# Performance work log

Measured on AMD Instinct MI355X. Metric: run time of the kernel, lower is better.

Reference implementation:

```python
import jax, jax.numpy as jnp
import numpy as np
import math

D = 384        # d_model
DC = 1024      # d_cut3r
NH = 8         # n_heads
NP = 4         # n_points
B, H, W = 8, 64, 64
EPS = 1e-5


def _offset_bias():
    thetas = np.arange(NH) * (2.0 * math.pi / NH)
    g = np.stack([np.cos(thetas), np.sin(thetas)], -1)
    g = g / np.abs(g).max(-1, keepdims=True)
    g = np.tile(g[:, None, :], (1, NP, 1)) * ((np.arange(NP) + 1.0) / NP)[None, :, None]
    return jnp.asarray(g.reshape(-1), jnp.float32)


def _ln(x, g, b):
    m = x.mean(-1, keepdims=True)
    v = ((x - m) ** 2).mean(-1, keepdims=True)
    return (x - m) * jax.lax.rsqrt(v + EPS) * g + b


def _grid_sample(img, grid):
    # img: [N, C, Hk, Wk]; grid: [N, Q, P, 2] with (x, y) in [-1, 1]
    # torch F.grid_sample semantics: bilinear, padding_mode='zeros', align_corners=False
    N, C, Hk, Wk = img.shape
    ix = ((grid[..., 0] + 1.0) * Wk - 1.0) * 0.5   # [N,Q,P] pixel coords
    iy = ((grid[..., 1] + 1.0) * Hk - 1.0) * 0.5
    x0 = jnp.floor(ix); y0 = jnp.floor(iy)
    wx1 = ix - x0; wx0 = 1.0 - wx1
    wy1 = iy - y0; wy0 = 1.0 - wy1
    flat = img.reshape(N, C, Hk * Wk)

    def corner(xf, yf, wgt):
        valid = (xf >= 0) & (xf < Wk) & (yf >= 0) & (yf < Hk)
        xi = jnp.clip(xf, 0, Wk - 1).astype(jnp.int32)
        yi = jnp.clip(yf, 0, Hk - 1).astype(jnp.int32)
        idx = (yi * Wk + xi).reshape(N, 1, -1)  # [N,1,Q*P]
        v = jnp.take_along_axis(flat, jnp.broadcast_to(idx, (N, C, idx.shape[-1])), axis=2)
        v = v.reshape(N, C, xf.shape[1], xf.shape[2])               # [N,C,Q,P]
        w = (wgt * valid.astype(img.dtype))[:, None]                # [N,1,Q,P]
        return v * w

    return (corner(x0, y0, wx0 * wy0) + corner(x0 + 1.0, y0, wx1 * wy0)
            + corner(x0, y0 + 1.0, wx0 * wy1) + corner(x0 + 1.0, y0 + 1.0, wx1 * wy1))


def setup_inputs() -> dict:
    key = jax.random.key(0)
    ks = jax.random.split(key, 16)
    rn = lambda k, shape: jax.random.normal(k, shape, jnp.float32) * 0.02
    return {
        'visual_feat': jax.random.normal(ks[0], (B, D, H, W), jnp.float32),
        'cut3r_features': jax.random.normal(ks[1], (B, 730, DC), jnp.float32),
        'ln_v_g': jnp.ones((D,), jnp.float32), 'ln_v_b': jnp.zeros((D,), jnp.float32),
        'ln_c_g': jnp.ones((DC,), jnp.float32), 'ln_c_b': jnp.zeros((DC,), jnp.float32),
        'W_c1': rn(ks[2], (DC, 2 * D)), 'b_c1': jnp.zeros((2 * D,), jnp.float32),
        'W_c2': rn(ks[3], (2 * D, D)), 'b_c2': jnp.zeros((D,), jnp.float32),
        'W_off': rn(ks[4], (D, NH * NP * 2)), 'b_off': _offset_bias(),
        'W_attn': rn(ks[5], (D, NH * NP)), 'b_attn': jnp.zeros((NH * NP,), jnp.float32),
        'W_out': rn(ks[6], (D, D)), 'b_out': jnp.zeros((D,), jnp.float32),
        'W_f1': rn(ks[7], (D, 4 * D)), 'b_f1': jnp.zeros((4 * D,), jnp.float32),
        'W_f2': rn(ks[8], (4 * D, D)), 'b_f2': jnp.zeros((D,), jnp.float32),
        'W_g1': rn(ks[9], (D, D // 4)), 'b_g1': jnp.zeros((D // 4,), jnp.float32),
        'W_g2': rn(ks[10], (D // 4, 1)), 'b_g2': jnp.full((1,), -5.0, jnp.float32),
        'ln_o_g': jnp.ones((D,), jnp.float32), 'ln_o_b': jnp.zeros((D,), jnp.float32),
    }


def reference(visual_feat, cut3r_features, ln_v_g, ln_v_b, ln_c_g, ln_c_b,
              W_c1, b_c1, W_c2, b_c2, W_off, b_off, W_attn, b_attn,
              W_out, b_out, W_f1, b_f1, W_f2, b_f2, W_g1, b_g1, W_g2, b_g2,
              ln_o_g, ln_o_b):
    Bb, C, Hh, Ww = visual_feat.shape
    Nq = Hh * Ww
    dh = C // NH
    vflat = visual_feat.reshape(Bb, C, Nq).transpose(0, 2, 1)            # [B,Nq,C]
    vn = _ln(vflat, ln_v_g, ln_v_b)
    cn = _ln(cut3r_features, ln_c_g, ln_c_b)
    cp = jax.nn.gelu(cn @ W_c1 + b_c1, approximate=False) @ W_c2 + b_c2  # [B,730,C]
    grid = cp[:, 1:, :].reshape(Bb, 27, 27, C).transpose(0, 3, 1, 2)     # [B,C,27,27]
    off = (vn @ W_off + b_off).reshape(Bb, Nq, NH, NP, 2)
    aw = jax.nn.softmax((vn @ W_attn + b_attn).reshape(Bb, Nq, NH, NP), axis=-1)
    loc = 2.0 * jax.nn.sigmoid(off) - 1.0                                # [-1,1]
    loc = loc.transpose(0, 2, 1, 3, 4).reshape(Bb * NH, Nq, NP, 2)
    value = grid.reshape(Bb * NH, dh, 27, 27)
    samp = _grid_sample(value, loc).reshape(Bb, NH, dh, Nq, NP)
    out = (samp * aw.transpose(0, 2, 1, 3)[:, :, None]).sum(-1)          # [B,NH,dh,Nq]
    out = out.transpose(0, 3, 1, 2).reshape(Bb, Nq, C)
    attn_out = out @ W_out + b_out
    ffn = jax.nn.gelu(attn_out @ W_f1 + b_f1, approximate=False) @ W_f2 + b_f2
    gate = jax.nn.sigmoid(jax.nn.relu(vflat @ W_g1 + b_g1) @ W_g2 + b_g2)  # [B,Nq,1]
    fused = _ln(vflat + gate * ffn, ln_o_g, ln_o_b)
    fused = fused.transpose(0, 2, 1).reshape(Bb, C, Hh, Ww)
    return fused, gate
```

## Files before the change

kernel.cpp:

```cpp
#include <hip/hip_runtime.h>
#include <hip/hip_bf16.h>
#include <math.h>

#define B_   8
#define D_   384
#define DC_  1024
#define NH_  8
#define NP_  4
#define DH_  48
#define NQ_  4096
#define NT_  730
#define NG_  729
#define GW_  27

typedef unsigned short u16;
typedef __attribute__((ext_vector_type(8))) short s8bf;
typedef __attribute__((ext_vector_type(4))) float f32x4;

__device__ __forceinline__ float bf2f(u16 u) { return __uint_as_float(((unsigned)u) << 16); }
__device__ __forceinline__ u16 f2bf(float f) {
    __hip_bfloat16 h = __float2bfloat16(f);
    return *reinterpret_cast<u16*>(&h);
}
__device__ __forceinline__ float rd(const float* p) { return *p; }
__device__ __forceinline__ float rd(const u16* p)   { return bf2f(*p); }
__device__ __forceinline__ void  wr(float* p, float v) { *p = v; }
__device__ __forceinline__ void  wr(u16* p, float v)   { *p = f2bf(v); }
__device__ __forceinline__ void fmacc4(float4& o, const float4 v, float w) {
    o.x = fmaf(v.x, w, o.x); o.y = fmaf(v.y, w, o.y);
    o.z = fmaf(v.z, w, o.z); o.w = fmaf(v.w, w, o.w);
}
__device__ __forceinline__ int imin(int a, int b) { return a < b ? a : b; }
__device__ __forceinline__ float fast_gelu(float x) {
    float z = 1.5957691216057308f * fmaf(0.044715f * x, x * x, x);
    return x / (1.f + __expf(-z));
}
__device__ __forceinline__ float fast_sigmoid(float x) {
    return 1.f / (1.f + __expf(-x));
}

#define GLOAD16(gp, lp) \
    __builtin_amdgcn_global_load_lds( \
        (const __attribute__((address_space(1))) void*)(gp), \
        (__attribute__((address_space(3))) void*)(lp), 16, 0, 0)

__global__ __launch_bounds__(256) void tr_ln_kernel(
    const float* __restrict__ visual,
    const float* __restrict__ g, const float* __restrict__ be,
    u16* __restrict__ vflat, u16* __restrict__ vn)
{
    __shared__ float lds[D_][33];
    __shared__ float sM[32], sR[32];
    const int blk = blockIdx.x;
    const int b = blk >> 7, q0 = (blk & 127) << 5;
    const int t = threadIdx.x;
    const int tx = t & 31, ty = t >> 5;
    const float* vb = visual + (size_t)b * D_ * NQ_ + q0;
#pragma unroll
    for (int ct = 0; ct < 12; ++ct)
#pragma unroll
        for (int i = 0; i < 32; i += 8) {
            const int c = ct * 32 + ty + i;
            lds[c][tx] = vb[(size_t)c * NQ_ + tx];
        }
    __syncthreads();
    const int wv = t >> 6, lane = t & 63;
    for (int k = 0; k < 8; ++k) {
        const int q = wv * 8 + k;
        float s = 0.f, ss = 0.f;
#pragma unroll
        for (int e = 0; e < 6; ++e) {
            float v = lds[lane * 6 + e][q];
            s += v; ss += v * v;
        }
#pragma unroll
        for (int o = 32; o > 0; o >>= 1) { s += __shfl_down(s, o); ss += __shfl_down(ss, o); }
        if (lane == 0) {
            float m = s / (float)D_;
            sM[q] = m; sR[q] = rsqrtf(ss / (float)D_ - m * m + 1e-5f);
        }
    }
    __syncthreads();
    for (int idx = t; idx < 32 * D_; idx += 256) {
        const int q = idx / D_, c = idx % D_;
        const float raw = lds[c][q];
        const size_t row = (size_t)b * NQ_ + q0 + q;
        vflat[row * D_ + c] = f2bf(raw);
        vn[row * D_ + c]    = f2bf((raw - sM[q]) * sR[q] * g[c] + be[c]);
    }
}

__global__ __launch_bounds__(256) void fused_ln_tr_kernel(
    const u16* __restrict__ vflat, const float* __restrict__ gate,
    const u16* __restrict__ ffn,
    const float* __restrict__ g, const float* __restrict__ be,
    float* __restrict__ outT)
{
    __shared__ float buf[D_][33];
    __shared__ float sM[32], sR[32], sG[32];
    const int blk = blockIdx.x;
    const int b = blk >> 7, q0 = (blk & 127) << 5;
    const int t = threadIdx.x;
    const int tx = t & 31, ty = t >> 5;
    if (t < 32) sG[t] = gate[(size_t)b * NQ_ + q0 + t];
    __syncthreads();
    for (int idx = t; idx < 32 * D_; idx += 256) {
        const int q = idx / D_, c = idx % D_;
        const size_t row = (size_t)b * NQ_ + q0 + q;
        buf[c][q] = bf2f(vflat[row * D_ + c]) + sG[q] * bf2f(ffn[row * D_ + c]);
    }
    __syncthreads();
    const int wv = t >> 6, lane = t & 63;
    for (int k = 0; k < 8; ++k) {
        const int q = wv * 8 + k;
        float s = 0.f, ss = 0.f;
#pragma unroll
        for (int e = 0; e < 6; ++e) {
            float v = buf[lane * 6 + e][q];
            s += v; ss += v * v;
        }
#pragma unroll
        for (int o = 32; o > 0; o >>= 1) { s += __shfl_down(s, o); ss += __shfl_down(ss, o); }
        if (lane == 0) {
            float m = s / (float)D_;
            sM[q] = m; sR[q] = rsqrtf(ss / (float)D_ - m * m + 1e-5f);
        }
    }
    __syncthreads();
    float* ob = outT + (size_t)b * D_ * NQ_ + q0;
#pragma unroll
    for (int ct = 0; ct < 12; ++ct)
#pragma unroll
        for (int i = 0; i < 32; i += 8) {
            const int c = ct * 32 + ty + i;
            ob[(size_t)c * NQ_ + tx] = (buf[c][tx] - sM[tx]) * sR[tx] * g[c] + be[c];
        }
}

struct WtD { const float* src; u16* dst; int R; int C; int start; };
struct WtArgs { WtD d[8]; };

__global__ __launch_bounds__(256) void wt_convert_kernel(WtArgs a)
{
    __shared__ float tile[32][33];
    const int bt = blockIdx.x;
    int wi = 0;
#pragma unroll
    for (int k = 1; k < 8; ++k) if (bt >= a.d[k].start) wi = k;
    const float* src = a.d[wi].src;
    u16*         dst = a.d[wi].dst;
    const int R = a.d[wi].R, C = a.d[wi].C;
    const int local = bt - a.d[wi].start;
    const int tilesX = C >> 5;
    const int c0 = (local % tilesX) << 5;
    const int r0 = (local / tilesX) << 5;
    const int tx = threadIdx.x & 31, ty = threadIdx.x >> 5;
#pragma unroll
    for (int i = 0; i < 32; i += 8)
        tile[ty + i][tx] = src[(size_t)(r0 + ty + i) * C + c0 + tx];
    __syncthreads();
#pragma unroll
    for (int i = 0; i < 32; i += 8)
        dst[(size_t)(c0 + ty + i) * R + r0 + tx] = f2bf(tile[tx][ty + i]);
}

__global__ __launch_bounds__(256) void ln_kernel(
    const float* __restrict__ x, const float* __restrict__ g, const float* __restrict__ be,
    u16* __restrict__ out, int width)
{
    __shared__ float buf[1024];
    __shared__ float red[4][2];
    const size_t row = blockIdx.x;
    const float* xr = x + row * width;
    const int t = threadIdx.x;
    float s = 0.f, ss = 0.f;
    for (int i = t; i < width; i += 256) {
        float v = xr[i]; buf[i] = v; s += v; ss += v * v;
    }
#pragma unroll
    for (int o = 32; o > 0; o >>= 1) { s += __shfl_down(s, o); ss += __shfl_down(ss, o); }
    const int wave = t >> 6, lane = t & 63;
    if (lane == 0) { red[wave][0] = s; red[wave][1] = ss; }
    __syncthreads();
    if (t == 0) {
        float S = 0.f, SS = 0.f;
        for (int w = 0; w < 4; ++w) { S += red[w][0]; SS += red[w][1]; }
        float m = S / width;
        float v = SS / width - m * m;
        red[0][0] = m; red[0][1] = rsqrtf(v + 1e-5f);
    }
    __syncthreads();
    const float m = red[0][0], rs = red[0][1];
    u16* op = out + row * width;
    for (int i = t; i < width; i += 256)
        op[i] = f2bf((buf[i] - m) * rs * g[i] + be[i]);
}

template <int ACT, typename Tout>
__global__ __launch_bounds__(256) void mfma_gemm(
    const u16* __restrict__ A, const u16* __restrict__ Wt,
    const float* __restrict__ bias, Tout* __restrict__ C,
    int M, int N, int K)
{
    __shared__ __align__(16) u16 smem[16384];
    const int t    = threadIdx.x;
    const int m0   = blockIdx.x * 128;
    const int n0   = blockIdx.y * 128;
    const int lane = t & 63;
    const int wv   = t >> 6;
    const int wm   = (wv >> 1) * 64;
    const int wn   = (wv & 1) * 64;
    const int lr   = lane & 15;
    const int lks  = lane >> 4;

    const int nbase = wv * 64 + lane;
    const u16* aS[2]; const u16* bS[2];
#pragma unroll
    for (int j = 0; j < 2; ++j) {
        const int n   = j * 256 + nbase;
        const int row = n >> 2;
        const int src = (n & 3) ^ ((row >> 1) & 3);
        aS[j] = A  + (size_t)imin(m0 + row, M - 1) * K + src * 8;
        bS[j] = Wt + (size_t)imin(n0 + row, N - 1) * K + src * 8;
    }
    const int doff = (wv * 64) * 8;

    f32x4 acc[4][4] = {};
    const int nt = K >> 5;

#pragma unroll
    for (int j = 0; j < 2; ++j) {
        GLOAD16(aS[j], &smem[j * 2048 + doff]);
        GLOAD16(bS[j], &smem[4096 + j * 2048 + doff]);
    }
    if (nt > 1) {
#pragma unroll
        for (int j = 0; j < 2; ++j) {
            GLOAD16(aS[j] + 32, &smem[8192 + j * 2048 + doff]);
            GLOAD16(bS[j] + 32, &smem[8192 + 4096 + j * 2048 + doff]);
        }
    }

    for (int ti = 0; ti < nt; ++ti) {
        if (ti + 1 < nt) {
            asm volatile("s_waitcnt vmcnt(4)" ::: "memory");
        } else {
            asm volatile("s_waitcnt vmcnt(0)" ::: "memory");
        }
        __builtin_amdgcn_s_barrier();

        const int cb = (ti & 1) * 8192;
        const u16* Ab = &smem[cb];
        const u16* Bb = &smem[cb + 4096];
        s8bf af[4], bfr[4];
#pragma unroll
        for (int i = 0; i < 4; ++i) {
            const int ra = wm + i * 16 + lr;
            const int rb = wn + i * 16 + lr;
            af[i]  = *reinterpret_cast<const s8bf*>(
                &Ab[(size_t)((ra << 2) | (lks ^ ((ra >> 1) & 3))) * 8]);
            bfr[i] = *reinterpret_cast<const s8bf*>(
                &Bb[(size_t)((rb << 2) | (lks ^ ((rb >> 1) & 3))) * 8]);
        }
#pragma unroll
        for (int i = 0; i < 4; ++i)
#pragma unroll
            for (int j = 0; j < 4; ++j)
                acc[i][j] = __builtin_amdgcn_mfma_f32_16x16x32_bf16(af[i], bfr[j], acc[i][j], 0, 0, 0);

        __builtin_amdgcn_s_barrier();

        if (ti + 2 < nt) {
            const int k2 = (ti + 2) << 5;
#pragma unroll
            for (int j = 0; j < 2; ++j) {
                GLOAD16(aS[j] + k2, &smem[cb + j * 2048 + doff]);
                GLOAD16(bS[j] + k2, &smem[cb + 4096 + j * 2048 + doff]);
            }
        }
    }

    if constexpr (sizeof(Tout) == 2) {
        u16* Cs = smem;
#pragma unroll
        for (int i = 0; i < 4; ++i)
#pragma unroll
            for (int j = 0; j < 4; ++j) {
                const int col = wn + j * 16 + lr;
                const float bb = bias[n0 + col];
#pragma unroll
                for (int r = 0; r < 4; ++r) {
                    const int row = wm + i * 16 + (lane >> 4) * 4 + r;
                    float v = acc[i][j][r] + bb;
                    if (ACT == 1) v = fast_gelu(v);
                    if (ACT == 2) v = v > 0.f ? v : 0.f;
                    const int xr = ((((row >> 2) & 3) ^ (row & 3)) << 4);
                    Cs[(row << 7) | (col ^ xr)] = f2bf(v);
                }
            }
        __syncthreads();
        u16* Cp = reinterpret_cast<u16*>(C);
#pragma unroll
        for (int it = 0; it < 8; ++it) {
            const int row = (t >> 4) + it * 16;
            const int gr  = m0 + row;
            const int q   = (t & 15) * 8;
            const int xr  = ((((row >> 2) & 3) ^ (row & 3)) << 4);
            s8bf v = *reinterpret_cast<const s8bf*>(&Cs[(row << 7) | (q ^ xr)]);
            if (gr < M)
                *reinterpret_cast<s8bf*>(Cp + (size_t)gr * N + n0 + q) = v;
        }
    } else {
#pragma unroll
        for (int i = 0; i < 4; ++i) {
            const int gr0 = m0 + wm + i * 16 + (lane >> 4) * 4;
#pragma unroll
            for (int j = 0; j < 4; ++j) {
                const int gc = n0 + wn + j * 16 + lr;
                if (gc >= N) continue;
                const float bb = bias[gc];
#pragma unroll
                for (int r = 0; r < 4; ++r) {
                    const int gr = gr0 + r;
                    if (gr >= M) continue;
                    float v = acc[i][j][r] + bb;
                    if (ACT == 1) v = fast_gelu(v);
                    if (ACT == 2) v = v > 0.f ? v : 0.f;
                    wr(C + (size_t)gr * N + gc, v);
                }
            }
        }
    }
}

template <int ACT>
__global__ __launch_bounds__(512) void mfma_gemm_wide(
    const u16* __restrict__ A, const u16* __restrict__ Wt,
    const float* __restrict__ bias, u16* __restrict__ C,
    int M, int N, int K)
{
    __shared__ __align__(16) u16 smem[32768];
    const int t    = threadIdx.x;
    const int m0   = blockIdx.x * 128;
    const int n0   = blockIdx.y * 256;
    const int lane = t & 63;
    const int wv   = t >> 6;
    const int wm   = (wv >> 2) * 64;
    const int wn   = (wv & 3) * 64;
    const int lr   = lane & 15;
    const int lks  = lane >> 4;

    const int nA = wv * 64 + lane;
    const int rA = nA >> 2, kA = (nA & 3) ^ ((rA >> 1) & 3);
    const u16* aS = A + (size_t)imin(m0 + rA, M - 1) * K + kA * 8;
    const u16* bS[2];
#pragma unroll
    for (int j = 0; j < 2; ++j) {
        const int n   = j * 512 + wv * 64 + lane;
        const int row = n >> 2;
        const int src = (n & 3) ^ ((row >> 1) & 3);
        bS[j] = Wt + (size_t)(n0 + row) * K + src * 8;
    }
    const int dA = (wv * 64) * 8;

    f32x4 acc[4][4] = {};
    const int nt = K >> 5;

    GLOAD16(aS, &smem[dA]);
#pragma unroll
    for (int j = 0; j < 2; ++j)
        GLOAD16(bS[j], &smem[4096 + (j * 512 + wv * 64) * 8]);
    if (nt > 1) {
        GLOAD16(aS + 32, &smem[12288 + dA]);
#pragma unroll
        for (int j = 0; j < 2; ++j)
            GLOAD16(bS[j] + 32, &smem[12288 + 4096 + (j * 512 + wv * 64) * 8]);
    }

    for (int ti = 0; ti < nt; ++ti) {
        if (ti + 1 < nt) {
            asm volatile("s_waitcnt vmcnt(3)" ::: "memory");
        } else {
            asm volatile("s_waitcnt vmcnt(0)" ::: "memory");
        }
        __builtin_amdgcn_s_barrier();

        const int cb = (ti & 1) * 12288;
        const u16* Ab = &smem[cb];
        const u16* Bb = &smem[cb + 4096];
        s8bf af[4], bfr[4];
#pragma unroll
        for (int i = 0; i < 4; ++i) {
            const int ra = wm + i * 16 + lr;
            const int rb = wn + i * 16 + lr;
            af[i]  = *reinterpret_cast<const s8bf*>(
                &Ab[(size_t)((ra << 2) | (lks ^ ((ra >> 1) & 3))) * 8]);
            bfr[i] = *reinterpret_cast<const s8bf*>(
                &Bb[(size_t)((rb << 2) | (lks ^ ((rb >> 1) & 3))) * 8]);
        }
#pragma unroll
        for (int i = 0; i < 4; ++i)
#pragma unroll
            for (int j = 0; j < 4; ++j)
                acc[i][j] = __builtin_amdgcn_mfma_f32_16x16x32_bf16(af[i], bfr[j], acc[i][j], 0, 0, 0);

        __builtin_amdgcn_s_barrier();

        if (ti + 2 < nt) {
            const int k2 = (ti + 2) << 5;
            GLOAD16(aS + k2, &smem[cb + dA]);
#pragma unroll
            for (int j = 0; j < 2; ++j)
                GLOAD16(bS[j] + k2, &smem[cb + 4096 + (j * 512 + wv * 64) * 8]);
        }
    }

    u16* Cs = smem;
#pragma unroll
    for (int i = 0; i < 4; ++i)
#pragma unroll
        for (int j = 0; j < 4; ++j) {
            const int col = wn + j * 16 + lr;
            const float bb = bias[n0 + col];
#pragma unroll
            for (int r = 0; r < 4; ++r) {
                const int row = wm + i * 16 + (lane >> 4) * 4 + r;
                float v = acc[i][j][r] + bb;
                if (ACT == 1) v = fast_gelu(v);
                if (ACT == 2) v = v > 0.f ? v : 0.f;
                const int xr = ((((row >> 2) & 3) ^ (row & 3)) << 4);
                Cs[(row << 8) | (col ^ xr)] = f2bf(v);
            }
        }
    __syncthreads();
#pragma unroll
    for (int it = 0; it < 8; ++it) {
        const int row = (t >> 5) + it * 16;
        const int gr  = m0 + row;
        const int q   = (t & 31) * 8;
        const int xr  = ((((row >> 2) & 3) ^ (row & 3)) << 4);
        s8bf v = *reinterpret_cast<const s8bf*>(&Cs[(row << 8) | (q ^ xr)]);
        if (gr < M)
            *reinterpret_cast<s8bf*>(C + (size_t)gr * N + n0 + q) = v;
    }
}

__global__ __launch_bounds__(128) void concat_bias_kernel(
    const float* __restrict__ b_off, const float* __restrict__ b_attn,
    float* __restrict__ b_cat)
{
    const int t = threadIdx.x;
    if (t < 64) b_cat[t] = b_off[t];
    else if (t < 96) b_cat[t] = b_attn[t - 64];
}

__global__ __launch_bounds__(256) void sample_kernel(
    const float* __restrict__ proj, const float* __restrict__ cpf,
    u16* __restrict__ out)
{
    __shared__ float4 sW[8][32];
    __shared__ int4   sT[8][32];

    const int blk = blockIdx.x;
    const int b   = blk / (NQ_ / 8);
    const int q0  = (blk % (NQ_ / 8)) * 8;
    const int t   = threadIdx.x;

    {
        const int qq = t >> 5, i = t & 31;
        const int h = i >> 2, p = i & 3;
        const size_t row = (size_t)b * NQ_ + q0 + qq;
        const float* pr = proj + row * 96;
        const float* lg = pr + 64 + h * 4;
        float l0 = lg[0], l1 = lg[1], l2 = lg[2], l3 = lg[3];
        float mx = fmaxf(fmaxf(l0, l1), fmaxf(l2, l3));
        float e0 = __expf(l0 - mx), e1 = __expf(l1 - mx);
        float e2 = __expf(l2 - mx), e3 = __expf(l3 - mx);
        float lp = (p == 0) ? l0 : (p == 1) ? l1 : (p == 2) ? l2 : l3;
        float aw = __expf(lp - mx) / (e0 + e1 + e2 + e3);
        float ox = pr[2 * i], oy = pr[2 * i + 1];
        float gx = 2.f * fast_sigmoid(ox) - 1.f;
        float gy = 2.f * fast_sigmoid(oy) - 1.f;
        float ix = ((gx + 1.f) * (float)GW_ - 1.f) * 0.5f;
        float iy = ((gy + 1.f) * (float)GW_ - 1.f) * 0.5f;
        float x0f = floorf(ix), y0f = floorf(iy);
        float wx1 = ix - x0f, wy1 = iy - y0f;
        float wx0 = 1.f - wx1, wy0 = 1.f - wy1;
        int xi = (int)x0f, yi = (int)y0f;
        bool vx0 = (xi >= 0) & (xi < GW_), vx1 = (xi + 1 >= 0) & (xi + 1 < GW_);
        bool vy0 = (yi >= 0) & (yi < GW_), vy1 = (yi + 1 >= 0) & (yi + 1 < GW_);
        float4 w;
        w.x = (vx0 & vy0) ? aw * wx0 * wy0 : 0.f;
        w.y = (vx1 & vy0) ? aw * wx1 * wy0 : 0.f;
        w.z = (vx0 & vy1) ? aw * wx0 * wy1 : 0.f;
        w.w = (vx1 & vy1) ? aw * wx1 * wy1 : 0.f;
        int cx0 = xi < 0 ? 0 : (xi > GW_ - 1 ? GW_ - 1 : xi);
        int cx1 = xi + 1 < 0 ? 0 : (xi + 1 > GW_ - 1 ? GW_ - 1 : xi + 1);
        int cy0 = yi < 0 ? 0 : (yi > GW_ - 1 ? GW_ - 1 : yi);
        int cy1 = yi + 1 < 0 ? 0 : (yi + 1 > GW_ - 1 ? GW_ - 1 : yi + 1);
        int4 tk;
        tk.x = cy0 * GW_ + cx0; tk.y = cy0 * GW_ + cx1;
        tk.z = cy1 * GW_ + cx0; tk.w = cy1 * GW_ + cx1;
        sW[qq][i] = w; sT[qq][i] = tk;
    }
    __syncthreads();

    const float4* vb4 = reinterpret_cast<const float4*>(cpf + (size_t)b * NT_ * D_ + D_);
    for (int idx = t; idx < 8 * 96; idx += 256) {
        const int qq = idx / 96, c4 = idx % 96, h = c4 / 12;
        float4 o = make_float4(0.f, 0.f, 0.f, 0.f);
#pragma unroll
        for (int p = 0; p < NP_; ++p) {
            const int i = h * 4 + p;
            const int4   tk = sT[qq][i];
            const float4 w  = sW[qq][i];
            fmacc4(o, vb4[(size_t)tk.x * 96 + c4], w.x);
            fmacc4(o, vb4[(size_t)tk.y * 96 + c4], w.y);
            fmacc4(o, vb4[(size_t)tk.z * 96 + c4], w.z);
            fmacc4(o, vb4[(size_t)tk.w * 96 + c4], w.w);
        }
        ushort4 pk;
        pk.x = f2bf(o.x); pk.y = f2bf(o.y); pk.z = f2bf(o.z); pk.w = f2bf(o.w);
        *reinterpret_cast<ushort4*>(&out[((size_t)b * NQ_ + q0 + qq) * D_ + c4 * 4]) = pk;
    }
}

__global__ __launch_bounds__(256) void gate_reduce_kernel(
    const float* __restrict__ gh, const float* __restrict__ Wg2,
    const float* __restrict__ bg2, float* __restrict__ gate_out)
{
    const int wave = threadIdx.x >> 6, lane = threadIdx.x & 63;
    const size_t row = (size_t)blockIdx.x * 4 + wave;
    const float* h = gh + row * 96;
    float s = h[lane] * Wg2[lane];
    if (lane < 32) s += h[64 + lane] * Wg2[64 + lane];
#pragma unroll
    for (int o = 32; o > 0; o >>= 1) s += __shfl_down(s, o);
    if (lane == 0) gate_out[row] = 1.f / (1.f + expf(-(s + bg2[0])));
}

extern "C" void kernel_launch(void* const* d_in, const int* in_sizes, int n_in,
                              void* d_out, int out_size, void* d_ws, size_t ws_size,
                              hipStream_t stream)
{
    const float* visual = (const float*)d_in[0];
    const float* cut3r  = (const float*)d_in[1];
    const float* ln_v_g = (const float*)d_in[2];
    const float* ln_v_b = (const float*)d_in[3];
    const float* ln_c_g = (const float*)d_in[4];
    const float* ln_c_b = (const float*)d_in[5];
    const float* W_c1 = (const float*)d_in[6];
    const float* b_c1 = (const float*)d_in[7];
    const float* W_c2 = (const float*)d_in[8];
    const float* b_c2 = (const float*)d_in[9];
    const float* W_off = (const float*)d_in[10];
    const float* b_off = (const float*)d_in[11];
    const float* W_attn = (const float*)d_in[12];
    const float* b_attn = (const float*)d_in[13];
    const float* W_out = (const float*)d_in[14];
    const float* b_out = (const float*)d_in[15];
    const float* W_f1 = (const float*)d_in[16];
    const float* b_f1 = (const float*)d_in[17];
    const float* W_f2 = (const float*)d_in[18];
    const float* b_f2 = (const float*)d_in[19];
    const float* W_g1 = (const float*)d_in[20];
    const float* b_g1 = (const float*)d_in[21];
    const float* W_g2 = (const float*)d_in[22];
    const float* b_g2 = (const float*)d_in[23];
    const float* ln_o_g = (const float*)d_in[24];
    const float* ln_o_b = (const float*)d_in[25];

    char* ws = (char*)d_ws;
    u16*   vflat   = (u16*)(ws + 0);
    u16*   vn      = (u16*)(ws + 25165824);
    u16*   attn_out= (u16*)(ws + 25165824);
    u16*   chid    = (u16*)(ws + 50331648);
    u16*   dout    = (u16*)(ws + 50331648);
    u16*   ffn     = (u16*)(ws + 50331648);
    float* cpf     = (float*)(ws + 75497472);
    u16*   wt_f1b  = (u16*)(ws + 84467712);
    u16*   wt_f2b  = wt_f1b + 589824;

    float* dout_f   = (float*)d_out;
    u16*   cn       = (u16*)d_out;
    float* proj_buf = dout_f;
    float* b_cat    = dout_f + 3145728;
    float* gate_hid = dout_f;
    u16*   hidden   = (u16*)d_out;
    char*  wtp      = (char*)d_out + 25165824;
    u16* wt_c1   = (u16*)wtp;
    u16* wt_c2   = wt_c1 + 786432;
    u16* wt_out  = wt_c2 + 294912;
    u16* wt_g1   = wt_out + 147456;
    u16* wt_off  = wt_g1 + 36864;
    u16* wt_attn = wt_off + 24576;
    float* out_fused = dout_f;
    float* out_gate  = dout_f + (size_t)B_ * D_ * NQ_;

    WtArgs wa;
    int cum = 0;
    auto fill = [&](int i, const float* src, u16* dst, int R, int C) {
        wa.d[i].src = src; wa.d[i].dst = dst; wa.d[i].R = R; wa.d[i].C = C;
        wa.d[i].start = cum; cum += (R >> 5) * (C >> 5);
    };
    fill(0, W_c1,  wt_c1,  1024, 768);
    fill(1, W_c2,  wt_c2,  768,  384);
    fill(2, W_out, wt_out, 384,  384);
    fill(3, W_g1,  wt_g1,  384,  96);
    fill(4, W_off, wt_off, 384,  64);
    fill(5, W_attn,wt_attn,384,  32);
    fill(6, W_f1,  wt_f1b, 384,  1536);
    fill(7, W_f2,  wt_f2b, 1536, 384);
    hipLaunchKernelGGL(wt_convert_kernel, dim3(cum), dim3(256), 0, stream, wa);
    hipLaunchKernelGGL(concat_bias_kernel, dim3(1), dim3(128), 0, stream, b_off, b_attn, b_cat);

    hipLaunchKernelGGL(tr_ln_kernel, dim3(1024), dim3(256), 0, stream,
                       visual, ln_v_g, ln_v_b, vflat, vn);
    hipLaunchKernelGGL(ln_kernel, dim3(5840), dim3(256), 0, stream,
                       cut3r, ln_c_g, ln_c_b, cn, 1024);
    hipLaunchKernelGGL((mfma_gemm<1, u16>), dim3(46, 6), dim3(256), 0, stream,
                       cn, wt_c1, b_c1, chid, 5840, 768, 1024);
    hipLaunchKernelGGL((mfma_gemm<0, float>), dim3(46, 3), dim3(256), 0, stream,
                       chid, wt_c2, b_c2, cpf, 5840, 384, 768);
    hipLaunchKernelGGL((mfma_gemm<0, float>), dim3(256, 1), dim3(256), 0, stream,
                       vn, wt_off, b_cat, proj_buf, 32768, 96, 384);
    hipLaunchKernelGGL(sample_kernel, dim3(4096), dim3(256), 0, stream,
                       proj_buf, cpf, dout);
    hipLaunchKernelGGL((mfma_gemm<0, u16>), dim3(256, 3), dim3(256), 0, stream,
                       dout, wt_out, b_out, attn_out, 32768, 384, 384);
    hipLaunchKernelGGL((mfma_gemm<2, float>), dim3(256, 1), dim3(256), 0, stream,
                       vflat, wt_g1, b_g1, gate_hid, 32768, 96, 384);
    hipLaunchKernelGGL(gate_reduce_kernel, dim3(8192), dim3(256), 0, stream,
                       gate_hid, W_g2, b_g2, out_gate);
    for (int c = 0; c < 2; ++c) {
        hipLaunchKernelGGL((mfma_gemm_wide<1>), dim3(128, 6), dim3(512), 0, stream,
                           attn_out + (size_t)c * 16384 * 384, wt_f1b, b_f1, hidden,
                           16384, 1536, 384);
        hipLaunchKernelGGL((mfma_gemm<0, u16>), dim3(128, 3), dim3(256), 0, stream,
                           hidden, wt_f2b, b_f2, ffn + (size_t)c * 16384 * 384,
                           16384, 384, 1536);
    }
    hipLaunchKernelGGL(fused_ln_tr_kernel, dim3(1024), dim3(256), 0, stream,
                       vflat, out_gate, ffn, ln_o_g, ln_o_b, out_fused);
}
```

Measured before the change: 345.1 us.

## Store sampling value grid in bf16 and gather 8 channels per load

The cut3r projection GEMM now writes its output in bf16 instead of fp32. The deformable sampling kernel reads that grid with 16-byte loads of 8 bf16 channels and issues all 16 corner loads up front, accumulating into two separate register sets. Each block now handles 16 queries instead of 8, halving the grid size. This halves the gather bandwidth and adds memory-level parallelism, at the cost of rounding the value grid to bf16 and using more registers per thread.

```diff
diff --git a/kernel.cpp b/kernel.cpp
--- a/kernel.cpp
+++ b/kernel.cpp
@@ -26,9 +26,10 @@
 __device__ __forceinline__ float rd(const u16* p)   { return bf2f(*p); }
 __device__ __forceinline__ void  wr(float* p, float v) { *p = v; }
 __device__ __forceinline__ void  wr(u16* p, float v)   { *p = f2bf(v); }
-__device__ __forceinline__ void fmacc4(float4& o, const float4 v, float w) {
-    o.x = fmaf(v.x, w, o.x); o.y = fmaf(v.y, w, o.y);
-    o.z = fmaf(v.z, w, o.z); o.w = fmaf(v.w, w, o.w);
+__device__ __forceinline__ void fmacc8(float* o, s8bf v, float w) {
+#pragma unroll
+    for (int k = 0; k < 8; ++k)
+        o[k] = fmaf(bf2f((u16)v[k]), w, o[k]);
 }
 __device__ __forceinline__ int imin(int a, int b) { return a < b ? a : b; }
 __device__ __forceinline__ float fast_gelu(float x) {
@@ -455,19 +456,19 @@
 }
 
 __global__ __launch_bounds__(256) void sample_kernel(
-    const float* __restrict__ proj, const float* __restrict__ cpf,
+    const float* __restrict__ proj, const u16* __restrict__ cpf16,
     u16* __restrict__ out)
 {
-    __shared__ float4 sW[8][32];
-    __shared__ int4   sT[8][32];
+    __shared__ float4 sW[16][32];
+    __shared__ int4   sT[16][32];
 
     const int blk = blockIdx.x;
-    const int b   = blk / (NQ_ / 8);
-    const int q0  = (blk % (NQ_ / 8)) * 8;
+    const int b   = blk / (NQ_ / 16);
+    const int q0  = (blk % (NQ_ / 16)) * 16;
     const int t   = threadIdx.x;
 
-    {
-        const int qq = t >> 5, i = t & 31;
+    for (int it = t; it < 16 * 32; it += 256) {
+        const int qq = it >> 5, i = it & 31;
         const int h = i >> 2, p = i & 3;
         const size_t row = (size_t)b * NQ_ + q0 + qq;
         const float* pr = proj + row * 96;
@@ -505,23 +506,35 @@
     }
     __syncthreads();
 
-    const float4* vb4 = reinterpret_cast<const float4*>(cpf + (size_t)b * NT_ * D_ + D_);
-    for (int idx = t; idx < 8 * 96; idx += 256) {
-        const int qq = idx / 96, c4 = idx % 96, h = c4 / 12;
-        float4 o = make_float4(0.f, 0.f, 0.f, 0.f);
-#pragma unroll
-        for (int p = 0; p < NP_; ++p) {
-            const int i = h * 4 + p;
-            const int4   tk = sT[qq][i];
-            const float4 w  = sW[qq][i];
-            fmacc4(o, vb4[(size_t)tk.x * 96 + c4], w.x);
-            fmacc4(o, vb4[(size_t)tk.y * 96 + c4], w.y);
-            fmacc4(o, vb4[(size_t)tk.z * 96 + c4], w.z);
-            fmacc4(o, vb4[(size_t)tk.w * 96 + c4], w.w);
-        }
-        ushort4 pk;
-        pk.x = f2bf(o.x); pk.y = f2bf(o.y); pk.z = f2bf(o.z); pk.w = f2bf(o.w);
-        *reinterpret_cast<ushort4*>(&out[((size_t)b * NQ_ + q0 + qq) * D_ + c4 * 4]) = pk;
+    const s8bf* vb8 = reinterpret_cast<const s8bf*>(cpf16 + (size_t)b * NT_ * D_ + D_);
+    for (int idx = t; idx < 16 * 48; idx += 256) {
+        const int qq = idx / 48, c8 = idx % 48, h = c8 / 6;
+        int4   tk0 = sT[qq][h * 4 + 0], tk1 = sT[qq][h * 4 + 1];
+        int4   tk2 = sT[qq][h * 4 + 2], tk3 = sT[qq][h * 4 + 3];
+        float4 w0  = sW[qq][h * 4 + 0], w1  = sW[qq][h * 4 + 1];
+        float4 w2  = sW[qq][h * 4 + 2], w3  = sW[qq][h * 4 + 3];
+        s8bf v00 = vb8[(size_t)tk0.x * 48 + c8], v01 = vb8[(size_t)tk0.y * 48 + c8];
+        s8bf v02 = vb8[(size_t)tk0.z * 48 + c8], v03 = vb8[(size_t)tk0.w * 48 + c8];
+        s8bf v10 = vb8[(size_t)tk1.x * 48 + c8], v11 = vb8[(size_t)tk1.y * 48 + c8];
+        s8bf v12 = vb8[(size_t)tk1.z * 48 + c8], v13 = vb8[(size_t)tk1.w * 48 + c8];
+        s8bf v20 = vb8[(size_t)tk2.x * 48 + c8], v21 = vb8[(size_t)tk2.y * 48 + c8];
+        s8bf v22 = vb8[(size_t)tk2.z * 48 + c8], v23 = vb8[(size_t)tk2.w * 48 + c8];
+        s8bf v30 = vb8[(size_t)tk3.x * 48 + c8], v31 = vb8[(size_t)tk3.y * 48 + c8];
+        s8bf v32 = vb8[(size_t)tk3.z * 48 + c8], v33 = vb8[(size_t)tk3.w * 48 + c8];
+        float oA[8] = {0.f,0.f,0.f,0.f,0.f,0.f,0.f,0.f};
+        float oB[8] = {0.f,0.f,0.f,0.f,0.f,0.f,0.f,0.f};
+        fmacc8(oA, v00, w0.x); fmacc8(oB, v01, w0.y);
+        fmacc8(oA, v02, w0.z); fmacc8(oB, v03, w0.w);
+        fmacc8(oA, v10, w1.x); fmacc8(oB, v11, w1.y);
+        fmacc8(oA, v12, w1.z); fmacc8(oB, v13, w1.w);
+        fmacc8(oA, v20, w2.x); fmacc8(oB, v21, w2.y);
+        fmacc8(oA, v22, w2.z); fmacc8(oB, v23, w2.w);
+        fmacc8(oA, v30, w3.x); fmacc8(oB, v31, w3.y);
+        fmacc8(oA, v32, w3.z); fmacc8(oB, v33, w3.w);
+        s8bf pk;
+#pragma unroll
+        for (int k = 0; k < 8; ++k) pk[k] = (short)f2bf(oA[k] + oB[k]);
+        *reinterpret_cast<s8bf*>(&out[((size_t)b * NQ_ + q0 + qq) * D_ + c8 * 8]) = pk;
     }
 }
 
@@ -577,7 +590,7 @@
     u16*   chid    = (u16*)(ws + 50331648);
     u16*   dout    = (u16*)(ws + 50331648);
     u16*   ffn     = (u16*)(ws + 50331648);
-    float* cpf     = (float*)(ws + 75497472);
+    u16*   cpf16   = (u16*)(ws + 75497472);
     u16*   wt_f1b  = (u16*)(ws + 84467712);
     u16*   wt_f2b  = wt_f1b + 589824;
 
@@ -620,12 +633,12 @@
                        cut3r, ln_c_g, ln_c_b, cn, 1024);
     hipLaunchKernelGGL((mfma_gemm<1, u16>), dim3(46, 6), dim3(256), 0, stream,
                        cn, wt_c1, b_c1, chid, 5840, 768, 1024);
-    hipLaunchKernelGGL((mfma_gemm<0, float>), dim3(46, 3), dim3(256), 0, stream,
-                       chid, wt_c2, b_c2, cpf, 5840, 384, 768);
+    hipLaunchKernelGGL((mfma_gemm<0, u16>), dim3(46, 3), dim3(256), 0, stream,
+                       chid, wt_c2, b_c2, cpf16, 5840, 384, 768);
     hipLaunchKernelGGL((mfma_gemm<0, float>), dim3(256, 1), dim3(256), 0, stream,
                        vn, wt_off, b_cat, proj_buf, 32768, 96, 384);
-    hipLaunchKernelGGL(sample_kernel, dim3(4096), dim3(256), 0, stream,
-                       proj_buf, cpf, dout);
+    hipLaunchKernelGGL(sample_kernel, dim3(2048), dim3(256), 0, stream,
+                       proj_buf, cpf16, dout);
     hipLaunchKernelGGL((mfma_gemm<0, u16>), dim3(256, 3), dim3(256), 0, stream,
                        dout, wt_out, b_out, attn_out, 32768, 384, 384);
     hipLaunchKernelGGL((mfma_gemm<2, float>), dim3(256, 1), dim3(256), 0, stream,
```

After: 327.3 us. 5.1% less time.
